# Performance work log

Hardware: AMD Instinct MI355X
Metric: run time of the kernel (lower is better)

The kernel has to match this reference:

```python
import jax, jax.numpy as jnp
import numpy as np

NUM_HEADS = 8
NUM_GROUPS = 32
EPS = 1e-5
RESCALE = 1.0


def setup_inputs() -> dict:
    key = jax.random.key(0)
    ks = jax.random.split(key, 7)
    b, c, h, w = 16, 512, 32, 32
    return {
        "x": jax.random.normal(ks[0], (b, c, h, w), jnp.float32),
        "norm_w": jax.random.normal(ks[1], (c,), jnp.float32),
        "norm_b": jax.random.normal(ks[2], (c,), jnp.float32),
        "qkv_w": jax.random.normal(ks[3], (3 * c, c), jnp.float32) * (c ** -0.5),
        "qkv_b": jax.random.normal(ks[4], (3 * c,), jnp.float32) * 0.02,
        "proj_w": jax.random.normal(ks[5], (c, c), jnp.float32) * (c ** -0.5),
        "proj_b": jax.random.normal(ks[6], (c,), jnp.float32) * 0.02,
    }


def _group_norm(x, w, b):
    # x: [B, C, L]
    B, C, L = x.shape
    g = x.reshape(B, NUM_GROUPS, (C // NUM_GROUPS) * L)
    mu = jnp.mean(g, axis=-1, keepdims=True)
    var = jnp.var(g, axis=-1, keepdims=True)
    g = (g - mu) * jax.lax.rsqrt(var + EPS)
    return g.reshape(B, C, L) * w[None, :, None] + b[None, :, None]


def reference(x, norm_w, norm_b, qkv_w, qkv_b, proj_w, proj_b):
    b, c, hh, ww = x.shape
    L = hh * ww
    H = NUM_HEADS
    ch = c // H  # head dim

    xr = x.reshape(b, c, L)
    hid = _group_norm(xr, norm_w, norm_b)

    # 1x1 conv1d == matmul over channel dim: [3c, c] @ [b, c, L]
    qkv = jnp.einsum('oc,bcl->bol', qkv_w, hid) + qkv_b[None, :, None]
    # torch: reshape(b*H, 3*ch, L).split(ch) -> per-head contiguous [q|k|v] blocks
    qkv = qkv.reshape(b, H, 3, ch, L)
    q, k, v = qkv[:, :, 0], qkv[:, :, 1], qkv[:, :, 2]  # [b, H, ch, L]

    scale = 1.0 / (ch ** 0.25)
    weight = jnp.einsum('bhct,bhcs->bhts', q * scale, k * scale)
    weight = jax.nn.softmax(weight.astype(jnp.float32), axis=-1).astype(weight.dtype)
    a = jnp.einsum('bhts,bhcs->bhct', weight, v)  # [b, H, ch, L]

    h = a.reshape(b, c, L)
    h = jnp.einsum('oc,bcl->bol', proj_w, h) + proj_b[None, :, None]
    h = h.reshape(b, c, hh, ww)
    return (x + h) / RESCALE
```

## Files before the change

kernel.cpp:

```cpp
#include <hip/hip_runtime.h>
#include <hip/hip_bf16.h>
#include <stdint.h>


using f32x4  = __attribute__((ext_vector_type(4))) float;
using bf16x8 = __attribute__((ext_vector_type(8))) __bf16;
using s8v    = __attribute__((ext_vector_type(8))) short;
using s4v    = __attribute__((ext_vector_type(4))) short;

__device__ __forceinline__ short f2bf(float f){
  union { float f; unsigned u; } c; c.f = f;
  unsigned r = (c.u + 0x7FFFu + ((c.u >> 16) & 1u)) >> 16;
  return (short)r;
}

__device__ __forceinline__ float exp2_fast(float x){
#if __has_builtin(__builtin_amdgcn_exp2f)
  return __builtin_amdgcn_exp2f(x);
#else
  return exp2f(x);
#endif
}

__device__ __forceinline__ void gl_lds16(const void* g, void* l){
  __builtin_amdgcn_global_load_lds((const __attribute__((address_space(1))) void*)g,
                                   (__attribute__((address_space(3))) void*)l, 16, 0, 0);
}

__global__ __launch_bounds__(256) void k_pre(const float* __restrict__ x,
                                             const float* __restrict__ w,
                                             const float* __restrict__ bia,
                                             short* __restrict__ hid,
                                             const float* __restrict__ qw,
                                             const float* __restrict__ pw,
                                             const float* __restrict__ qb,
                                             short* __restrict__ qwb,
                                             short* __restrict__ pwb,
                                             float* __restrict__ qbp){
  int bid = blockIdx.x;
  int tid = threadIdx.x;
  if (bid >= 512){
    int i = (bid - 512) * 256 + tid;
    if (i < 786432){
      int o = i >> 9, kk = i & 511;
      int h = o / 192, rem = o - h*192;
      int nr = (rem >> 6)*512 + h*64 + (rem & 63);
      qwb[nr*512 + kk] = f2bf(qw[i]);
    } else if (i < 1048576){
      int j = i - 786432;
      pwb[j] = f2bf(pw[j]);
    } else if (i < 1050112){
      int o = i - 1048576;
      int h = o / 192, rem = o - h*192;
      qbp[(rem >> 6)*512 + h*64 + (rem & 63)] = qb[o];
    }
    return;
  }
  int b = bid >> 5;
  int g = bid & 31;
  const float* xg = x + ((size_t)b*512 + g*16)*1024;
  int l0 = tid * 4;
  float v[16][4];
  float s1 = 0.f, s2 = 0.f;
  #pragma unroll
  for (int c = 0; c < 16; c++){
    f32x4 t = *(const f32x4*)(xg + c*1024 + l0);
    #pragma unroll
    for (int j = 0; j < 4; j++){ v[c][j] = t[j]; s1 += t[j]; s2 += t[j]*t[j]; }
  }
  #pragma unroll
  for (int m = 32; m; m >>= 1){ s1 += __shfl_xor(s1, m); s2 += __shfl_xor(s2, m); }
  __shared__ float r1[4], r2[4];
  int wv = tid >> 6, ln = tid & 63;
  if (ln == 0){ r1[wv] = s1; r2[wv] = s2; }
  __syncthreads();
  s1 = r1[0]+r1[1]+r1[2]+r1[3];
  s2 = r2[0]+r2[1]+r2[2]+r2[3];
  float mu = s1 * (1.f/16384.f);
  float var = s2 * (1.f/16384.f) - mu*mu;
  float rs = rsqrtf(var + 1e-5f);
  float ww[16], bb[16];
  #pragma unroll
  for (int c = 0; c < 16; c++){ ww[c] = w[g*16+c]*rs; bb[c] = bia[g*16+c]; }
  #pragma unroll
  for (int j = 0; j < 4; j++){
    short o[16];
    #pragma unroll
    for (int c = 0; c < 16; c++) o[c] = f2bf((v[c][j]-mu)*ww[c] + bb[c]);
    short* dst = hid + ((size_t)(b*1024 + l0 + j))*512 + g*16;
    *(s8v*)dst     = *(s8v*)o;
    *(s8v*)(dst+8) = *(s8v*)(o+8);
  }
}

__global__ __launch_bounds__(256) void k_gemmQ(
    const short* __restrict__ A, const short* __restrict__ Bm,
    const float* __restrict__ bias,
    short* __restrict__ q_t, short* __restrict__ k_t, short* __restrict__ v_t)
{
  __shared__ short Al[2][128*64];
  __shared__ short Bl[2][128*64];
  int id = blockIdx.x;
  int xcd = id & 7, ix = id >> 3;
  int mt = ix % 12, nt = ix / 12;
  int m0 = mt * 128;
  int n0 = (xcd + 8*nt) * 128;
  int tid = threadIdx.x;
  int lane = tid & 63;
  int wv = tid >> 6;
  int wr = wv >> 1, wc = wv & 1;
  int l15 = lane & 15, g = lane >> 4;
  f32x4 acc[4][4] = {};

  auto STAGE = [&](int db, int t){
    int k0 = t * 64;
    #pragma unroll
    for (int i = 0; i < 8; i++){
      int cc = wv*8 + i;
      if (cc < 16){
        int slot = cc*64 + lane;
        int row = slot >> 3, off = slot & 7;
        gl_lds16(A + (size_t)(m0+row)*512 + k0 + (off ^ (row&7))*8,
                 (char*)Al[db] + cc*1024);
      } else {
        int slot = (cc-16)*64 + lane;
        int row = slot >> 3, off = slot & 7;
        gl_lds16(Bm + (size_t)(n0+row)*512 + k0 + (off ^ (row&7))*8,
                 (char*)Bl[db] + (cc-16)*1024);
      }
    }
  };

  auto COMPUTE = [&](int db){
    #pragma unroll
    for (int kk = 0; kk < 2; kk++){
      bf16x8 af[4], bf[4];
      #pragma unroll
      for (int m = 0; m < 4; m++){
        int row = wr*64 + m*16 + l15;
        int byte = row*128 + (((kk*64) + (g*16)) ^ ((row&7)<<4));
        af[m] = *(const bf16x8*)((char*)Al[db] + byte);
      }
      #pragma unroll
      for (int n = 0; n < 4; n++){
        int row = wc*64 + n*16 + l15;
        int byte = row*128 + (((kk*64) + (g*16)) ^ ((row&7)<<4));
        bf[n] = *(const bf16x8*)((char*)Bl[db] + byte);
      }
      __builtin_amdgcn_s_setprio(1);
      #pragma unroll
      for (int m = 0; m < 4; m++)
        #pragma unroll
        for (int n = 0; n < 4; n++)
          acc[m][n] = __builtin_amdgcn_mfma_f32_16x16x32_bf16(af[m], bf[n], acc[m][n], 0, 0, 0);
      __builtin_amdgcn_s_setprio(0);
    }
  };

  STAGE(0, 0);
  for (int t = 0; t < 8; t++){
    __syncthreads();
    if (t < 7) STAGE((t+1)&1, t+1);
    COMPUTE(t&1);
  }
  __syncthreads();

  int sel = m0 >> 9;
  if (sel < 2){
    const float sc = (sel == 0) ? 0.18033688011112042f : 1.0f;
    short* dstb = (sel == 0) ? q_t : k_t;
    #pragma unroll
    for (int m = 0; m < 4; m++){
      int ob = m0 + wr*64 + m*16 + (g<<2);
      int hh = (ob>>6)&7, c0 = ob&63;
      float bs[4];
      #pragma unroll
      for (int r = 0; r < 4; r++) bs[r] = bias[ob+r];
      #pragma unroll
      for (int n = 0; n < 4; n++){
        int nn = n0 + wc*64 + n*16 + l15;
        int bb = nn >> 10, ll = nn & 1023;
        int bh = bb*8 + hh;
        short o4[4];
        #pragma unroll
        for (int r = 0; r < 4; r++) o4[r] = f2bf((acc[m][n][r] + bs[r]) * sc);
        *(s4v*)(dstb + ((size_t)bh*1024 + ll)*64 + c0) = *(s4v*)o4;
      }
    }
  } else {
    short* Sc = (short*)Al;
    #pragma unroll
    for (int m = 0; m < 4; m++){
      int ob = m0 + wr*64 + m*16 + (g<<2);
      int h2 = (ob>>6)&1, cq = (ob>>4)&3;
      float bs[4];
      #pragma unroll
      for (int r = 0; r < 4; r++) bs[r] = bias[ob+r];
      #pragma unroll
      for (int n = 0; n < 4; n++){
        int nn = n0 + wc*64 + n*16 + l15;
        int sl = nn & 63, sreg = (nn>>6)&1;
        int ks2 = sl >> 5, gq = (sl>>2)&3, i2 = (sl&3) + 4*((sl>>4)&1);
        int base = (h2*2 + sreg)*4096 + (((ks2*4+gq)*4 + cq)*16 + (g<<2))*8 + i2;
        #pragma unroll
        for (int r = 0; r < 4; r++)
          Sc[base + r*8] = f2bf(acc[m][n][r] + bs[r]);
      }
    }
    __syncthreads();
    int b0  = n0 >> 10;
    int s64 = (n0 >> 6) & 15;
    int hb  = (m0 - 1024) >> 6;
    #pragma unroll
    for (int it = 0; it < 8; it++){
      int flat = it*2048 + tid*8;
      int h2 = flat >> 13, rem = flat & 8191, sreg = rem >> 12, off = rem & 4095;
      int bh = b0*8 + hb + h2;
      *(s8v*)(v_t + ((size_t)bh*16 + s64 + sreg)*4096 + off) = *(const s8v*)(Sc + flat);
    }
  }
}

__global__ __launch_bounds__(256) void k_gemmP(
    const short* __restrict__ A, const short* __restrict__ Bm,
    const float* __restrict__ bias, const float* __restrict__ xres,
    float* __restrict__ outp)
{
  __shared__ short Al[2][128*64];
  __shared__ short Bl[2][128*64];
  int id = blockIdx.x;
  int xcd = id & 7, ix = id >> 3;
  int mt = ix & 3, nt = ix >> 2;
  int m0 = mt * 128;
  int n0 = (xcd + 8*nt) * 128;
  int tid = threadIdx.x;
  int lane = tid & 63;
  int wv = tid >> 6;
  int wr = wv >> 1, wc = wv & 1;
  int l15 = lane & 15, g = lane >> 4;
  f32x4 acc[4][4] = {};

  auto STAGE = [&](int db, int t){
    int k0 = t * 64;
    #pragma unroll
    for (int i = 0; i < 8; i++){
      int cc = wv*8 + i;
      if (cc < 16){
        int slot = cc*64 + lane;
        int row = slot >> 3, off = slot & 7;
        gl_lds16(A + (size_t)(m0+row)*512 + k0 + (off ^ (row&7))*8,
                 (char*)Al[db] + cc*1024);
      } else {
        int slot = (cc-16)*64 + lane;
        int row = slot >> 3, off = slot & 7;
        gl_lds16(Bm + (size_t)(n0+row)*512 + k0 + (off ^ (row&7))*8,
                 (char*)Bl[db] + (cc-16)*1024);
      }
    }
  };

  auto COMPUTE = [&](int db){
    #pragma unroll
    for (int kk = 0; kk < 2; kk++){
      bf16x8 af[4], bf[4];
      #pragma unroll
      for (int m = 0; m < 4; m++){
        int row = wr*64 + m*16 + l15;
        int byte = row*128 + (((kk*64) + (g*16)) ^ ((row&7)<<4));
        af[m] = *(const bf16x8*)((char*)Al[db] + byte);
      }
      #pragma unroll
      for (int n = 0; n < 4; n++){
        int row = wc*64 + n*16 + l15;
        int byte = row*128 + (((kk*64) + (g*16)) ^ ((row&7)<<4));
        bf[n] = *(const bf16x8*)((char*)Bl[db] + byte);
      }
      __builtin_amdgcn_s_setprio(1);
      #pragma unroll
      for (int m = 0; m < 4; m++)
        #pragma unroll
        for (int n = 0; n < 4; n++)
          acc[m][n] = __builtin_amdgcn_mfma_f32_16x16x32_bf16(af[m], bf[n], acc[m][n], 0, 0, 0);
      __builtin_amdgcn_s_setprio(0);
    }
  };

  STAGE(0, 0);
  for (int t = 0; t < 8; t++){
    __syncthreads();
    if (t < 7) STAGE((t+1)&1, t+1);
    COMPUTE(t&1);
  }

  #pragma unroll
  for (int m = 0; m < 4; m++){
    int ob = m0 + wr*64 + m*16 + (g<<2);
    float bs[4];
    #pragma unroll
    for (int r = 0; r < 4; r++) bs[r] = bias[ob+r];
    #pragma unroll
    for (int n = 0; n < 4; n++){
      int nn = n0 + wc*64 + n*16 + l15;
      int bb = nn >> 10, ll = nn & 1023;
      #pragma unroll
      for (int r = 0; r < 4; r++){
        size_t idx = ((size_t)bb*512 + ob + r)*1024 + ll;
        outp[idx] = xres[idx] + acc[m][n][r] + bs[r];
      }
    }
  }
}

__global__ __launch_bounds__(256, 2) void k_attn(
    const short* __restrict__ q_t, const short* __restrict__ k_t,
    const short* __restrict__ v_t, short* __restrict__ a_bt)
{
  __shared__ short Kh[4*2048];
  __shared__ short Vh[4*2048];
  int id = blockIdx.x;
  int xcd = id & 7, ix = id >> 3;
  int bh = xcd*16 + (ix >> 2);
  int qb = ix & 3;
  int bb = bh >> 3, hh = bh & 7;
  int tid = threadIdx.x;
  int lane = tid & 63;
  int wv = tid >> 6;
  int l15 = lane & 15, g = lane >> 4;

  bf16x8 qf[4][2];
  #pragma unroll
  for (int qt = 0; qt < 4; qt++){
    const short* qbase = q_t + ((size_t)bh*1024 + qb*256 + qt*64 + wv*16 + l15)*64 + g*8;
    qf[qt][0] = *(const bf16x8*)(qbase);
    qf[qt][1] = *(const bf16x8*)(qbase + 32);
  }
  asm volatile("" :: "v"(qf[0][0]), "v"(qf[0][1]), "v"(qf[1][0]), "v"(qf[1][1]),
                     "v"(qf[2][0]), "v"(qf[2][1]), "v"(qf[3][0]), "v"(qf[3][1]));

  bf16x8 onesb;
  #pragma unroll
  for (int i = 0; i < 8; i++) onesb[i] = (__bf16)1.0f;

  f32x4 o[4][4] = {};
  f32x4 osum[4] = {};

  auto STAGE = [&](int db, int h){
    int t64 = h >> 1, ks = h & 1;
    #pragma unroll
    for (int i = 0; i < 2; i++){
      int cc = wv*2 + i;
      if (cc < 4){
        int row = cc*8 + (lane>>3), slot = lane & 7;
        gl_lds16(k_t + ((size_t)bh*1024 + h*32 + row)*64 + ((slot ^ (row&7))*8),
                 (char*)Kh + db*4096 + cc*1024);
      } else {
        gl_lds16(v_t + ((size_t)bh*16 + t64)*4096 + ks*2048 + (cc-4)*512 + lane*8,
                 (char*)Vh + db*4096 + (cc-4)*1024);
      }
    }
  };

  auto COMPUTE = [&](int db){
    const char* Kb = (const char*)Kh + db*4096;
    const char* Vb = (const char*)Vh + db*4096;
    f32x4 scl[4][2] = {};
    #pragma unroll
    for (int jl = 0; jl < 2; jl++){
      int row = jl*16 + l15;
      int swz = (row&7)<<4;
      bf16x8 kf0 = *(const bf16x8*)(Kb + row*128 + ((g*16) ^ swz));
      bf16x8 kf1 = *(const bf16x8*)(Kb + row*128 + ((64 + g*16) ^ swz));
      __builtin_amdgcn_s_setprio(1);
      #pragma unroll
      for (int qt = 0; qt < 4; qt++){
        scl[qt][jl] = __builtin_amdgcn_mfma_f32_16x16x32_bf16(kf0, qf[qt][0], scl[qt][jl], 0, 0, 0);
        scl[qt][jl] = __builtin_amdgcn_mfma_f32_16x16x32_bf16(kf1, qf[qt][1], scl[qt][jl], 0, 0, 0);
      }
      __builtin_amdgcn_s_setprio(0);
    }
    bf16x8 pa[4];
    #pragma unroll
    for (int qt = 0; qt < 4; qt++){
      #pragma unroll
      for (int i2 = 0; i2 < 8; i2++)
        pa[qt][i2] = (__bf16)exp2_fast(scl[qt][i2>>2][i2&3]);
      osum[qt] = __builtin_amdgcn_mfma_f32_16x16x32_bf16(pa[qt], onesb, osum[qt], 0, 0, 0);
    }
    #pragma unroll
    for (int jd = 0; jd < 4; jd++){
      bf16x8 vbb = *(const bf16x8*)(Vb + (g*4+jd)*256 + l15*16);
      __builtin_amdgcn_s_setprio(1);
      #pragma unroll
      for (int qt = 0; qt < 4; qt++)
        o[qt][jd] = __builtin_amdgcn_mfma_f32_16x16x32_bf16(pa[qt], vbb, o[qt][jd], 0, 0, 0);
      __builtin_amdgcn_s_setprio(0);
    }
  };

  STAGE(0, 0);
  STAGE(1, 1);
  for (int h = 0; h < 30; h++){
    STAGE((h+2)&3, h+2);
    asm volatile("s_waitcnt vmcnt(4)" ::: "memory");
    __builtin_amdgcn_s_barrier();
    __builtin_amdgcn_sched_barrier(0);
    COMPUTE(h&3);
  }
  asm volatile("s_waitcnt vmcnt(2)" ::: "memory");
  __builtin_amdgcn_s_barrier();
  __builtin_amdgcn_sched_barrier(0);
  COMPUTE(2);
  asm volatile("s_waitcnt vmcnt(0)" ::: "memory");
  __builtin_amdgcn_s_barrier();
  __builtin_amdgcn_sched_barrier(0);
  COMPUTE(3);

  #pragma unroll
  for (int qt = 0; qt < 4; qt++){
    #pragma unroll
    for (int r = 0; r < 4; r++){
      float inv = 1.f / osum[qt][r];
      int qrow = qb*256 + qt*64 + wv*16 + g*4 + r;
      #pragma unroll
      for (int jd = 0; jd < 4; jd++)
        a_bt[((size_t)bb*1024 + qrow)*512 + hh*64 + jd*16 + l15] = f2bf(o[qt][jd][r] * inv);
    }
  }
}

extern "C" void kernel_launch(void* const* d_in, const int* in_sizes, int n_in,
                              void* d_out, int out_size, void* d_ws, size_t ws_size,
                              hipStream_t stream){
  const float* x  = (const float*)d_in[0];
  const float* nw = (const float*)d_in[1];
  const float* nb = (const float*)d_in[2];
  const float* qw = (const float*)d_in[3];
  const float* qb = (const float*)d_in[4];
  const float* pw = (const float*)d_in[5];
  const float* pb = (const float*)d_in[6];
  float* outp = (float*)d_out;

  char* ws = (char*)d_ws;
  short* hid  = (short*)(ws);
  short* qwb  = (short*)(ws + 16777216);
  short* pwb  = (short*)(ws + 18350080);
  short* q_t  = (short*)(ws + 18874368);
  short* k_t  = (short*)(ws + 35651584);
  short* v_t  = (short*)(ws + 52428800);
  short* a_bt = hid;
  float* qbp  = (float*)d_out;
  if (ws_size < 69206016) return;

  k_pre<<<4615, 256, 0, stream>>>(x, nw, nb, hid, qw, pw, qb, qwb, pwb, qbp);
  k_gemmQ<<<1536, 256, 0, stream>>>(qwb, hid, qbp, q_t, k_t, v_t);
  k_attn<<<512, 256, 0, stream>>>(q_t, k_t, v_t, a_bt);
  k_gemmP<<<512, 256, 0, stream>>>(pwb, a_bt, pb, x, outp);
}
```

Measured before the change: 119.6 us.

## Split attention into smaller query blocks and software-pipeline QK with exp/PV

The attention kernel now handles 128 query rows per block instead of 256, doubling the grid to 1024 blocks and raising the launch-bounds occupancy hint from 2 to 4. Its loop is restructured so the QK^T MFMAs for the next K tile are issued before the exp and PV work of the current tile, using two score buffers in alternation. Both GEMM kernels and the attention kernel now precompute their global-to-LDS staging pointers once rather than recomputing address arithmetic on every stage. The cost is K/V tiles being loaded twice as many times overall, plus register pressure from the dual score buffers under the tighter occupancy target.

Measured after the change: 115.3 us (median of 3 runs). -3.6%, faster.

```diff
diff --git a/kernel.cpp b/kernel.cpp
--- a/kernel.cpp
+++ b/kernel.cpp
@@ -112,23 +112,27 @@
   int l15 = lane & 15, g = lane >> 4;
   f32x4 acc[4][4] = {};
 
+  const short* srcp[8]; char* dstp[8];
+  #pragma unroll
+  for (int i = 0; i < 8; i++){
+    int cc = wv*8 + i;
+    if (cc < 16){
+      int slot = cc*64 + lane;
+      int row = slot >> 3, off = slot & 7;
+      srcp[i] = A + (size_t)(m0+row)*512 + (off ^ (row&7))*8;
+      dstp[i] = (char*)Al[0] + cc*1024;
+    } else {
+      int slot = (cc-16)*64 + lane;
+      int row = slot >> 3, off = slot & 7;
+      srcp[i] = Bm + (size_t)(n0+row)*512 + (off ^ (row&7))*8;
+      dstp[i] = (char*)Bl[0] + (cc-16)*1024;
+    }
+  }
+
   auto STAGE = [&](int db, int t){
-    int k0 = t * 64;
-    #pragma unroll
-    for (int i = 0; i < 8; i++){
-      int cc = wv*8 + i;
-      if (cc < 16){
-        int slot = cc*64 + lane;
-        int row = slot >> 3, off = slot & 7;
-        gl_lds16(A + (size_t)(m0+row)*512 + k0 + (off ^ (row&7))*8,
-                 (char*)Al[db] + cc*1024);
-      } else {
-        int slot = (cc-16)*64 + lane;
-        int row = slot >> 3, off = slot & 7;
-        gl_lds16(Bm + (size_t)(n0+row)*512 + k0 + (off ^ (row&7))*8,
-                 (char*)Bl[db] + (cc-16)*1024);
-      }
-    }
+    #pragma unroll
+    for (int i = 0; i < 8; i++)
+      gl_lds16(srcp[i] + t*64, dstp[i] + db*16384);
   };
 
   auto COMPUTE = [&](int db){
@@ -240,23 +244,27 @@
   int l15 = lane & 15, g = lane >> 4;
   f32x4 acc[4][4] = {};
 
+  const short* srcp[8]; char* dstp[8];
+  #pragma unroll
+  for (int i = 0; i < 8; i++){
+    int cc = wv*8 + i;
+    if (cc < 16){
+      int slot = cc*64 + lane;
+      int row = slot >> 3, off = slot & 7;
+      srcp[i] = A + (size_t)(m0+row)*512 + (off ^ (row&7))*8;
+      dstp[i] = (char*)Al[0] + cc*1024;
+    } else {
+      int slot = (cc-16)*64 + lane;
+      int row = slot >> 3, off = slot & 7;
+      srcp[i] = Bm + (size_t)(n0+row)*512 + (off ^ (row&7))*8;
+      dstp[i] = (char*)Bl[0] + (cc-16)*1024;
+    }
+  }
+
   auto STAGE = [&](int db, int t){
-    int k0 = t * 64;
-    #pragma unroll
-    for (int i = 0; i < 8; i++){
-      int cc = wv*8 + i;
-      if (cc < 16){
-        int slot = cc*64 + lane;
-        int row = slot >> 3, off = slot & 7;
-        gl_lds16(A + (size_t)(m0+row)*512 + k0 + (off ^ (row&7))*8,
-                 (char*)Al[db] + cc*1024);
-      } else {
-        int slot = (cc-16)*64 + lane;
-        int row = slot >> 3, off = slot & 7;
-        gl_lds16(Bm + (size_t)(n0+row)*512 + k0 + (off ^ (row&7))*8,
-                 (char*)Bl[db] + (cc-16)*1024);
-      }
-    }
+    #pragma unroll
+    for (int i = 0; i < 8; i++)
+      gl_lds16(srcp[i] + t*64, dstp[i] + db*16384);
   };
 
   auto COMPUTE = [&](int db){
@@ -311,7 +319,7 @@
   }
 }
 
-__global__ __launch_bounds__(256, 2) void k_attn(
+__global__ __launch_bounds__(256, 4) void k_attn(
     const short* __restrict__ q_t, const short* __restrict__ k_t,
     const short* __restrict__ v_t, short* __restrict__ a_bt)
 {
@@ -319,51 +327,56 @@
   __shared__ short Vh[4*2048];
   int id = blockIdx.x;
   int xcd = id & 7, ix = id >> 3;
-  int bh = xcd*16 + (ix >> 2);
-  int qb = ix & 3;
+  int bh = xcd*16 + (ix >> 3);
+  int qb = ix & 7;
   int bb = bh >> 3, hh = bh & 7;
   int tid = threadIdx.x;
   int lane = tid & 63;
   int wv = tid >> 6;
   int l15 = lane & 15, g = lane >> 4;
 
-  bf16x8 qf[4][2];
-  #pragma unroll
-  for (int qt = 0; qt < 4; qt++){
-    const short* qbase = q_t + ((size_t)bh*1024 + qb*256 + qt*64 + wv*16 + l15)*64 + g*8;
+  bf16x8 qf[2][2];
+  #pragma unroll
+  for (int qt = 0; qt < 2; qt++){
+    const short* qbase = q_t + ((size_t)bh*1024 + qb*128 + qt*64 + wv*16 + l15)*64 + g*8;
     qf[qt][0] = *(const bf16x8*)(qbase);
     qf[qt][1] = *(const bf16x8*)(qbase + 32);
   }
-  asm volatile("" :: "v"(qf[0][0]), "v"(qf[0][1]), "v"(qf[1][0]), "v"(qf[1][1]),
-                     "v"(qf[2][0]), "v"(qf[2][1]), "v"(qf[3][0]), "v"(qf[3][1]));
+  asm volatile("" :: "v"(qf[0][0]), "v"(qf[0][1]), "v"(qf[1][0]), "v"(qf[1][1]));
 
   bf16x8 onesb;
   #pragma unroll
   for (int i = 0; i < 8; i++) onesb[i] = (__bf16)1.0f;
 
-  f32x4 o[4][4] = {};
-  f32x4 osum[4] = {};
-
+  f32x4 o[2][4] = {};
+  f32x4 osum[2] = {};
+
+  const short* sp[2]; char* dp[2];
+  #pragma unroll
+  for (int i = 0; i < 2; i++){
+    int cc = wv*2 + i;
+    if (cc < 4){
+      int row = cc*8 + (lane>>3), slot = lane & 7;
+      sp[i] = k_t + ((size_t)bh*1024 + row)*64 + (slot ^ (row&7))*8;
+      dp[i] = (char*)Kh + cc*1024;
+    } else {
+      sp[i] = v_t + (size_t)bh*16*4096 + (cc-4)*512 + lane*8;
+      dp[i] = (char*)Vh + (cc-4)*1024;
+    }
+  }
   auto STAGE = [&](int db, int h){
-    int t64 = h >> 1, ks = h & 1;
-    #pragma unroll
-    for (int i = 0; i < 2; i++){
-      int cc = wv*2 + i;
-      if (cc < 4){
-        int row = cc*8 + (lane>>3), slot = lane & 7;
-        gl_lds16(k_t + ((size_t)bh*1024 + h*32 + row)*64 + ((slot ^ (row&7))*8),
-                 (char*)Kh + db*4096 + cc*1024);
-      } else {
-        gl_lds16(v_t + ((size_t)bh*16 + t64)*4096 + ks*2048 + (cc-4)*512 + lane*8,
-                 (char*)Vh + db*4096 + (cc-4)*1024);
-      }
-    }
-  };
-
-  auto COMPUTE = [&](int db){
+    #pragma unroll
+    for (int i = 0; i < 2; i++)
+      gl_lds16(sp[i] + h*2048, dp[i] + db*4096);
+  };
+
+  auto QK = [&](f32x4 (&scl)[2][2], int db){
     const char* Kb = (const char*)Kh + db*4096;
-    const char* Vb = (const char*)Vh + db*4096;
-    f32x4 scl[4][2] = {};
+    #pragma unroll
+    for (int qt = 0; qt < 2; qt++)
+      #pragma unroll
+      for (int jl = 0; jl < 2; jl++)
+        scl[qt][jl] = f32x4{0.f, 0.f, 0.f, 0.f};
     #pragma unroll
     for (int jl = 0; jl < 2; jl++){
       int row = jl*16 + l15;
@@ -372,15 +385,19 @@
       bf16x8 kf1 = *(const bf16x8*)(Kb + row*128 + ((64 + g*16) ^ swz));
       __builtin_amdgcn_s_setprio(1);
       #pragma unroll
-      for (int qt = 0; qt < 4; qt++){
+      for (int qt = 0; qt < 2; qt++){
         scl[qt][jl] = __builtin_amdgcn_mfma_f32_16x16x32_bf16(kf0, qf[qt][0], scl[qt][jl], 0, 0, 0);
         scl[qt][jl] = __builtin_amdgcn_mfma_f32_16x16x32_bf16(kf1, qf[qt][1], scl[qt][jl], 0, 0, 0);
       }
       __builtin_amdgcn_s_setprio(0);
     }
-    bf16x8 pa[4];
-    #pragma unroll
-    for (int qt = 0; qt < 4; qt++){
+  };
+
+  auto EXP_PV = [&](f32x4 (&scl)[2][2], int db){
+    const char* Vb = (const char*)Vh + db*4096;
+    bf16x8 pa[2];
+    #pragma unroll
+    for (int qt = 0; qt < 2; qt++){
       #pragma unroll
       for (int i2 = 0; i2 < 8; i2++)
         pa[qt][i2] = (__bf16)exp2_fast(scl[qt][i2>>2][i2&3]);
@@ -391,36 +408,47 @@
       bf16x8 vbb = *(const bf16x8*)(Vb + (g*4+jd)*256 + l15*16);
       __builtin_amdgcn_s_setprio(1);
       #pragma unroll
-      for (int qt = 0; qt < 4; qt++)
+      for (int qt = 0; qt < 2; qt++)
         o[qt][jd] = __builtin_amdgcn_mfma_f32_16x16x32_bf16(pa[qt], vbb, o[qt][jd], 0, 0, 0);
       __builtin_amdgcn_s_setprio(0);
     }
   };
 
+  f32x4 sA[2][2], sB[2][2];
+
   STAGE(0, 0);
   STAGE(1, 1);
-  for (int h = 0; h < 30; h++){
-    STAGE((h+2)&3, h+2);
-    asm volatile("s_waitcnt vmcnt(4)" ::: "memory");
-    __builtin_amdgcn_s_barrier();
-    __builtin_amdgcn_sched_barrier(0);
-    COMPUTE(h&3);
-  }
   asm volatile("s_waitcnt vmcnt(2)" ::: "memory");
   __builtin_amdgcn_s_barrier();
   __builtin_amdgcn_sched_barrier(0);
-  COMPUTE(2);
+  QK(sA, 0);
+  for (int h = 0; h < 30; h += 2){
+    STAGE((h+2)&3, h+2);
+    asm volatile("s_waitcnt vmcnt(2)" ::: "memory");
+    __builtin_amdgcn_s_barrier();
+    __builtin_amdgcn_sched_barrier(0);
+    QK(sB, (h+1)&3);
+    EXP_PV(sA, h&3);
+    STAGE((h+3)&3, h+3);
+    asm volatile("s_waitcnt vmcnt(2)" ::: "memory");
+    __builtin_amdgcn_s_barrier();
+    __builtin_amdgcn_sched_barrier(0);
+    QK(sA, (h+2)&3);
+    EXP_PV(sB, (h+1)&3);
+  }
   asm volatile("s_waitcnt vmcnt(0)" ::: "memory");
   __builtin_amdgcn_s_barrier();
   __builtin_amdgcn_sched_barrier(0);
-  COMPUTE(3);
-
-  #pragma unroll
-  for (int qt = 0; qt < 4; qt++){
+  QK(sB, 3);
+  EXP_PV(sA, 2);
+  EXP_PV(sB, 3);
+
+  #pragma unroll
+  for (int qt = 0; qt < 2; qt++){
     #pragma unroll
     for (int r = 0; r < 4; r++){
       float inv = 1.f / osum[qt][r];
-      int qrow = qb*256 + qt*64 + wv*16 + g*4 + r;
+      int qrow = qb*128 + qt*64 + wv*16 + g*4 + r;
       #pragma unroll
       for (int jd = 0; jd < 4; jd++)
         a_bt[((size_t)bb*1024 + qrow)*512 + hh*64 + jd*16 + l15] = f2bf(o[qt][jd][r] * inv);
@@ -453,6 +481,6 @@
 
   k_pre<<<4615, 256, 0, stream>>>(x, nw, nb, hid, qw, pw, qb, qwb, pwb, qbp);
   k_gemmQ<<<1536, 256, 0, stream>>>(qwb, hid, qbp, q_t, k_t, v_t);
-  k_attn<<<512, 256, 0, stream>>>(q_t, k_t, v_t, a_bt);
+  k_attn<<<1024, 256, 0, stream>>>(q_t, k_t, v_t, a_bt);
   k_gemmP<<<512, 256, 0, stream>>>(pwb, a_bt, pb, x, outp);
 }
```
